# Kernel tuning notes

Hardware: AMD Instinct MI355X
Metric: run time of the kernel (lower is better)

Reference implementation:

```python
import jax, jax.numpy as jnp
import numpy as np

B, SEQ, NVAR, DM, K = 2, 512, 64, 128, 2
SCALE = DM ** -0.5  # ScaledDotProductAttention scale, lsa=False so constant


def _period_branch(x4, Wel, bel, Wq, bq, Wk, bk, Wv, bv, Wo, bo, period):
    # x4: [B, DM(time), NVAR, DM(dim)] -- output of start_embed
    pad = (-DM) % period
    pn = (DM + pad) // period  # period_num
    xp = jnp.pad(x4, ((0, 0), (0, pad), (0, 0), (0, 0)))
    # torch .unfold(dim=1, size=period, step=period) -> [B, pn, NVAR, DM, period]
    xw = xp.reshape(B, pn, period, NVAR, DM).transpose(0, 1, 3, 4, 2)
    # emb_linear over the d_model (dim) axis
    xw = jnp.einsum('bqndl,ed->bqnel', xw, Wel) + bel[None, None, None, :, None]
    # -> [B, NVAR, dim, pn, period] then flatten to conv1d layout [bn, dim, L]
    X = xw.transpose(0, 2, 3, 1, 4).reshape(B * NVAR, DM, pn * period)
    # 1x1 Conv1d QKV projections over the channel (dim) axis
    q = jnp.einsum('bdl,ed->bel', X, Wq) + bq[None, :, None]
    k = jnp.einsum('bdl,ed->bel', X, Wk) + bk[None, :, None]
    v = jnp.einsum('bdl,ed->bel', X, Wv) + bv[None, :, None]
    q_s = q.reshape(B * NVAR, DM, pn, period).transpose(0, 1, 3, 2)  # [bn,dim,pl,pn]
    k_s = k.reshape(B * NVAR, DM, pn, period)                         # [bn,dim,pn,pl]
    v_s = v.reshape(B * NVAR, DM, pn, period).transpose(0, 1, 3, 2)  # [bn,dim,pl,pn]
    attn = jax.nn.softmax(jnp.einsum('bdip,bdpj->bdij', q_s, k_s) * SCALE, axis=-1)
    o = jnp.einsum('bdij,bdjp->bdip', attn, v_s)  # [bn, dim, period, pn]
    o = o.reshape(B * NVAR, DM, period * pn)[:, :, :DM]  # truncate to n_heads=DM
    return o @ Wo.T + bo  # to_out Linear(n_heads, n_heads), dropout eval-mode


def reference(x, W_emb, b_emb, W_start, b_start, Wel, bel, Wq, bq, Wk, bk, Wv, bv, Wo, bo, f1, f2):
    # inverted embedding: Linear(seq_len->d_model) over time, then permute -> [B, DM, NVAR]
    xe = (jnp.einsum('bsn,sd->bnd', x, W_emb) + b_emb).transpose(0, 2, 1)
    # FFT_for_Period amplitudes; top-k frequency indices f1,f2 are static (host-side in torch)
    amp = jnp.abs(jnp.fft.rfft(xe, axis=1)).mean(-1)  # [B, DM//2+1]
    pw = jax.nn.softmax(jnp.stack([amp[:, f1], amp[:, f2]], -1), axis=-1)  # [B, K]
    # start_embed: Linear(1 -> d_model) -> [B, DM, NVAR, DM]
    x4 = xe[..., None] * W_start + b_start
    outs = [_period_branch(x4, Wel, bel, Wq, bq, Wk, bk, Wv, bv, Wo, bo, DM // f)
            for f in (f1, f2)]
    res = jnp.stack(outs, -1)                      # [B*NVAR, DM, DM, K]
    pw_b = jnp.repeat(pw, NVAR, axis=0)            # [B*NVAR, K] (b-major order matches reshape)
    out = (res * pw_b[:, None, None, :]).sum(-1)
    return out.reshape(B, NVAR, DM, DM)


def setup_inputs() -> dict:
    key = jax.random.key(0)
    ks = jax.random.split(key, 16)
    s = 0.02
    d = {
        'x': jax.random.normal(ks[0], (B, SEQ, NVAR), jnp.float32),
        'W_emb': jax.random.normal(ks[1], (SEQ, DM), jnp.float32) * s,
        'b_emb': jax.random.normal(ks[2], (DM,), jnp.float32) * s,
        'W_start': jax.random.normal(ks[3], (DM,), jnp.float32) * s,
        'b_start': jax.random.normal(ks[4], (DM,), jnp.float32) * s,
        'Wel': jax.random.normal(ks[5], (DM, DM), jnp.float32) * s,
        'bel': jax.random.normal(ks[6], (DM,), jnp.float32) * s,
        'Wq': jax.random.normal(ks[7], (DM, DM), jnp.float32) * s,
        'bq': jax.random.normal(ks[8], (DM,), jnp.float32) * s,
        'Wk': jax.random.normal(ks[9], (DM, DM), jnp.float32) * s,
        'bk': jax.random.normal(ks[10], (DM,), jnp.float32) * s,
        'Wv': jax.random.normal(ks[11], (DM, DM), jnp.float32) * s,
        'bv': jax.random.normal(ks[12], (DM,), jnp.float32) * s,
        'Wo': jax.random.normal(ks[13], (DM, DM), jnp.float32) * s,
        'bo': jax.random.normal(ks[14], (DM,), jnp.float32) * s,
    }
    # host-side FFT period detection, mirroring torch's .detach().cpu().numpy() topk
    xe = np.einsum('bsn,sd->bnd', np.asarray(d['x']), np.asarray(d['W_emb'])) + np.asarray(d['b_emb'])
    xe = xe.transpose(0, 2, 1)  # [B, DM, NVAR]
    fl = np.abs(np.fft.rfft(xe, axis=1)).mean(0).mean(-1)
    fl[0] = 0.0
    top = np.argsort(-fl, kind='stable')[:K]
    d['f1'] = int(top[0])
    d['f2'] = int(top[1])
    return d
```

## Files before the change

kernel.cpp:

```cpp
#include <hip/hip_runtime.h>

#define DMD 128
#define NV 64
#define BB 2
#define SQ 512
#define NBN 128
#define ASCALE 0.08838834764831845f
#define L2E 1.4426950408889634f
#define CSC (ASCALE * L2E)

#define WS_XE  0
#define WS_PW  (WS_XE + NBN*DMD)
#define WS_VEC (WS_PW + 4)
#define WS_OB  (WS_VEC + 9*DMD)

__global__ __launch_bounds__(512) void k_xe(const float* __restrict__ x,
                                            const float* __restrict__ W_emb,
                                            const float* __restrict__ b_emb,
                                            float* __restrict__ ws) {
    int bn = blockIdx.x;
    int b = bn >> 6, n = bn & 63;
    int tid = threadIdx.x;
    int t = tid & 127, sc = tid >> 7;
    __shared__ float xsh[SQ];
    __shared__ float part[3][DMD];
    xsh[tid] = x[(b * SQ + tid) * NV + n];
    __syncthreads();
    float acc = 0.f;
    const float* W = W_emb + (sc * 128) * DMD + t;
#pragma unroll 8
    for (int s = 0; s < 128; ++s) acc = fmaf(xsh[sc * 128 + s], W[s * DMD], acc);
    if (sc) part[sc - 1][t] = acc;
    __syncthreads();
    if (sc == 0)
        ws[WS_XE + bn * DMD + t] = acc + part[0][t] + part[1][t] + part[2][t] + b_emb[t];
}

__global__ __launch_bounds__(128) void k_prep(const int* __restrict__ f1p,
                                              const int* __restrict__ f2p,
                                              const float* __restrict__ Wel, const float* __restrict__ bel,
                                              const float* __restrict__ W_start, const float* __restrict__ b_start,
                                              const float* __restrict__ Wq, const float* __restrict__ bq,
                                              const float* __restrict__ Wk, const float* __restrict__ bk,
                                              const float* __restrict__ Wv, const float* __restrict__ bv,
                                              float* __restrict__ ws) {
    int tid = threadIdx.x;
    __shared__ float ct[DMD], st[DMD];
    __shared__ float a2[2];
    __shared__ float A[DMD], C[DMD], BL[DMD];
    if (blockIdx.x < 2) {
        int b = blockIdx.x;
        float ang = (float)tid * 0.04908738521234052f;
        ct[tid] = cosf(ang);
        st[tid] = sinf(ang);
        __syncthreads();
        int k = tid >> 6;
        int n = tid & 63;
        int f = k ? f2p[0] : f1p[0];
        const float* xr = ws + WS_XE + (b * NV + n) * DMD;
        float re = 0.f, im = 0.f;
        for (int t = 0; t < DMD; ++t) {
            int ph = (f * t) & (DMD - 1);
            float v = xr[t];
            re = fmaf(v, ct[ph], re);
            im = fmaf(v, st[ph], im);
        }
        float amp = sqrtf(re * re + im * im);
        for (int off = 32; off > 0; off >>= 1) amp += __shfl_down(amp, off);
        if (n == 0) a2[k] = amp * (1.0f / NV);
        __syncthreads();
        if (tid == 0) {
            float m = fmaxf(a2[0], a2[1]);
            float e0 = expf(a2[0] - m), e1 = expf(a2[1] - m);
            float inv = 1.0f / (e0 + e1);
            ws[WS_PW + b * 2 + 0] = e0 * inv;
            ws[WS_PW + b * 2 + 1] = e1 * inv;
        }
    } else {
        int e = tid;
        float a = 0.f, c = 0.f;
        for (int d = 0; d < DMD; ++d) {
            float w = Wel[e * DMD + d];
            a = fmaf(w, W_start[d], a);
            c = fmaf(w, b_start[d], c);
        }
        A[e] = a;
        C[e] = c + bel[e];
        BL[e] = bel[e];
        __syncthreads();
        float aq = 0, cq = 0, pq = 0, ak = 0, ck = 0, pk = 0, av = 0, cv = 0, pv = 0;
        for (int d = 0; d < DMD; ++d) {
            float Ad = A[d], Cd = C[d], Bd = BL[d];
            float wq = Wq[e * DMD + d], wk = Wk[e * DMD + d], wv = Wv[e * DMD + d];
            aq = fmaf(wq, Ad, aq); cq = fmaf(wq, Cd, cq); pq = fmaf(wq, Bd, pq);
            ak = fmaf(wk, Ad, ak); ck = fmaf(wk, Cd, ck); pk = fmaf(wk, Bd, pk);
            av = fmaf(wv, Ad, av); cv = fmaf(wv, Cd, cv); pv = fmaf(wv, Bd, pv);
        }
        float* V = ws + WS_VEC;
        V[0 * DMD + e] = aq; V[1 * DMD + e] = cq + bq[e]; V[2 * DMD + e] = pq + bq[e];
        V[3 * DMD + e] = ak; V[4 * DMD + e] = ck + bk[e]; V[5 * DMD + e] = pk + bk[e];
        V[6 * DMD + e] = av; V[7 * DMD + e] = cv + bv[e]; V[8 * DMD + e] = pv + bv[e];
    }
}


template<int UH, int NP>
__device__ __forceinline__ void attn_pathA(
    int P, int pn, int r, int Prows, int e0, int br, float pwv,
    const float* __restrict__ V, const float* xs, const float* U,
    const float* xt, float (*obuf)[132], int tid)
{
    int lane4 = tid & 3;
    int i0 = tid >> 2;
    int jb = lane4 * UH;

    float Ur[UH], xtr[UH], xq0[UH], xq1[UH];
#pragma unroll
    for (int u = 0; u < UH; ++u) {
        int j = jb + u, jc = (j < P) ? j : 0;
        Ur[u] = U[jc];
        xtr[u] = xt[jc];
        xq0[u] = (j < DMD) ? xs[j] : 0.f;
        int i1 = P + j;
        xq1[u] = (i1 < DMD) ? xs[i1] : 0.f;
    }

    int nrep = (Prows > 32) ? 2 : 1;
    for (int rep = 0; rep < nrep; ++rep) {
        int i = i0 + rep * 32;
        bool rowact = (i < Prows);
        int ic = rowact ? i : 0;
        float xtic = xt[ic];
        bool rowvalid = (ic < r);

        float g[UH];
#pragma unroll
        for (int u = 0; u < UH; ++u) g[u] = 0.f;
        for (int p = 0; p < pn - 1; ++p) {
            float xi = xs[p * P + ic];
#pragma unroll
            for (int u = 0; u < UH; ++u) {
                int j = jb + u, jc = (j < P) ? j : 0;
                g[u] = fmaf(xi, xs[p * P + jc], g[u]);
            }
        }

        for (int ec = 0; ec < 8; ++ec) {
            int e = e0 + ec;
            float Aq = V[e],        Cq = V[DMD + e],   Pq = V[2 * DMD + e];
            float Ak = V[3 * DMD + e], Ck = V[4 * DMD + e], Pk = V[5 * DMD + e];
            float Av = V[6 * DMD + e], Cv = V[7 * DMD + e], Pv = V[8 * DMD + e];
            float c1 = CSC * Aq * Ak, c3 = CSC * Cq * Ak;
            float asi = CSC * (rowvalid ? fmaf(xtic, Aq, Cq) : Pq);

            float l0 = 0.f, l1 = 0.f, w0 = 0.f, w1 = 0.f;
            float accq[NP];
#pragma unroll
            for (int q = 0; q < NP; ++q) accq[q] = 0.f;

#pragma unroll
            for (int u = 0; u < UH; ++u) {
                int j = jb + u;
                float bK = (j < r) ? fmaf(xtr[u], Ak, Ck) : Pk;
                float S = fmaf(asi, bK, fmaf(c3, Ur[u], c1 * g[u]));
                float ev = exp2f(S);
                ev = (j < P) ? ev : 0.f;
                if (u & 1) l1 += ev; else l0 += ev;
                float evr = (j < r) ? ev : 0.f;
                if (u & 1) w1 += evr; else w0 += evr;
                accq[0] = fmaf(ev, xq0[u], accq[0]);
                if (NP >= 2) accq[1] = fmaf(ev, xq1[u], accq[1]);
#pragma unroll
                for (int q = 2; q < NP; ++q) {
                    int idx = q * P + j;
                    float xv = (idx < DMD) ? xs[idx] : 0.f;
                    accq[q] = fmaf(ev, xv, accq[q]);
                }
            }
            float l = l0 + l1, wr = w0 + w1;
            l += __shfl_xor(l, 1);  l += __shfl_xor(l, 2);
            wr += __shfl_xor(wr, 1); wr += __shfl_xor(wr, 2);
#pragma unroll
            for (int q = 0; q < NP; ++q) {
                if (q < pn) {
                    accq[q] += __shfl_xor(accq[q], 1);
                    accq[q] += __shfl_xor(accq[q], 2);
                }
            }
            if (lane4 == 0 && rowact) {
                float li = 1.f / l;
#pragma unroll
                for (int q = 0; q < NP; ++q) {
                    if (q < pn) {
                        int mo = i * pn + q;
                        if (mo < DMD) {
                            float o;
                            if (q == pn - 1) {
                                float sl = wr * li;
                                o = fmaf(Av, accq[q] * li, fmaf(Cv, sl, Pv * (1.f - sl)));
                            } else {
                                o = fmaf(Av, accq[q] * li, Cv);
                            }
                            float val = pwv * o;
                            if (br == 0) obuf[ec][mo] = val;
                            else         obuf[ec][mo] += val;
                        }
                    }
                }
            }
        }
    }
}

__device__ __forceinline__ void attn_pathB(
    int P, int pn, int r, int Prows, int e0, int br, float pwv,
    const float* __restrict__ V, const float* xs, const float* U,
    const float* xt, const float* G, float (*obuf)[132], int tid)
{
    int i2 = tid / pn, p2 = tid - i2 * pn;
    bool lastp = (p2 == pn - 1);
    bool rowvalid = (i2 < r);
    float xti = xt[i2];

    float Gr[16], xsr[16], Urr[16], xtr[16];
#pragma unroll
    for (int j = 0; j < 16; ++j) {
        int jc = (j < P) ? j : 0;
        Gr[j] = G[i2 * P + jc];
        Urr[j] = U[jc];
        xtr[j] = xt[jc];
        int idx = p2 * P + j;
        xsr[j] = (idx < DMD && j < P) ? xs[idx] : 0.f;
    }

    for (int ec = 0; ec < 8; ++ec) {
        int e = e0 + ec;
        float Aq = V[e],        Cq = V[DMD + e],   Pq = V[2 * DMD + e];
        float Ak = V[3 * DMD + e], Ck = V[4 * DMD + e], Pk = V[5 * DMD + e];
        float Av = V[6 * DMD + e], Cv = V[7 * DMD + e], Pv = V[8 * DMD + e];
        float c1 = CSC * Aq * Ak, c3 = CSC * Cq * Ak;
        float asi = CSC * (rowvalid ? fmaf(xti, Aq, Cq) : Pq);

        float l0 = 0.f, l1 = 0.f, w0 = 0.f, w1 = 0.f, a0 = 0.f, a1 = 0.f;
#pragma unroll
        for (int j = 0; j < 16; ++j) {
            float bK = (j < r) ? fmaf(xtr[j], Ak, Ck) : Pk;
            float S = fmaf(asi, bK, fmaf(c3, Urr[j], c1 * Gr[j]));
            float ev = exp2f(S);
            ev = (j < P) ? ev : 0.f;
            if (j & 1) l1 += ev; else l0 += ev;
            float evr = (j < r) ? ev : 0.f;
            if (j & 1) w1 += evr; else w0 += evr;
            if (j & 1) a1 = fmaf(ev, xsr[j], a1); else a0 = fmaf(ev, xsr[j], a0);
        }
        float l = l0 + l1, wr = w0 + w1, accx = a0 + a1;
        float li = 1.f / l;
        float o;
        if (lastp) { float sl = wr * li; o = fmaf(Av, accx * li, fmaf(Cv, sl, Pv * (1.f - sl))); }
        else       o = fmaf(Av, accx * li, Cv);
        float val = pwv * o;
        if (br == 0) obuf[ec][tid] = val;
        else         obuf[ec][tid] += val;
    }
}

__device__ __forceinline__ void attn_rank1(
    int e0, int br, float pwv, const float* __restrict__ V,
    const float* xs, float (*obuf)[132], int tid)
{
    float xi = xs[tid];
    float t[8], l[8], ax[8];
#pragma unroll
    for (int k = 0; k < 8; ++k) {
        int e = e0 + k;
        float Aq = V[e], Cq = V[DMD + e], Ak = V[3 * DMD + e];
        t[k] = CSC * fmaf(xi, Aq, Cq) * Ak;
        l[k] = 0.f; ax[k] = 0.f;
    }
#pragma unroll 4
    for (int j = 0; j < DMD; ++j) {
        float xj = xs[j];
#pragma unroll
        for (int k = 0; k < 8; ++k) {
            float ev = exp2f(t[k] * xj);
            l[k] += ev;
            ax[k] = fmaf(ev, xj, ax[k]);
        }
    }
#pragma unroll
    for (int k = 0; k < 8; ++k) {
        int e = e0 + k;
        float Av = V[6 * DMD + e], Cv = V[7 * DMD + e];
        float o = fmaf(Av, ax[k] / l[k], Cv);
        float val = pwv * o;
        if (br == 0) obuf[k][tid] = val;
        else         obuf[k][tid] += val;
    }
}

__global__ __launch_bounds__(128) void k_attn(const int* __restrict__ f1p,
                                              const int* __restrict__ f2p,
                                              float* __restrict__ ws) {
    int bn = blockIdx.y;
    int b = bn >> 6;
    int e0 = blockIdx.x * 8;
    int tid = threadIdx.x;

    __shared__ float xs[DMD], U[64], xt[64], G[256];
    __shared__ float obuf[8][132];

    xs[tid] = ws[WS_XE + bn * DMD + tid];
    int fv0 = f1p[0], fv1 = f2p[0];
    float pw0 = ws[WS_PW + b * 2 + 0];
    float pw1 = ws[WS_PW + b * 2 + 1];
    const float* V = ws + WS_VEC;
    __syncthreads();

    for (int br = 0; br < 2; ++br) {
        int f = br ? fv1 : fv0;
        float pwv = br ? pw1 : pw0;
        int P = DMD / f;
        int pn = (DMD + P - 1) / P;
        int r = DMD - (pn - 1) * P;
        int Prows = (DMD + pn - 1) / pn;

        if (br == 1) __syncthreads();

        if (P == DMD) {
            attn_rank1(e0, br, pwv, V, xs, obuf, tid);
        } else {
            if (tid < P) {
                float s = 0.f;
                for (int p = 0; p < pn - 1; ++p) s += xs[p * P + tid];
                U[tid] = s;
                xt[tid] = (tid < r) ? xs[(pn - 1) * P + tid] : 0.f;
            }
            if (P <= 16) {
                int tot = Prows * P;
                for (int idx = tid; idx < tot; idx += 128) {
                    int gi = idx / P, gj = idx - gi * P;
                    float s = 0.f;
                    for (int p = 0; p < pn - 1; ++p)
                        s = fmaf(xs[p * P + gi], xs[p * P + gj], s);
                    G[idx] = s;
                }
            }
            __syncthreads();

            if (P > 32) {
                if (pn == 2) attn_pathA<16, 2>(P, pn, r, Prows, e0, br, pwv, V, xs, U, xt, obuf, tid);
                else         attn_pathA<16, 4>(P, pn, r, Prows, e0, br, pwv, V, xs, U, xt, obuf, tid);
            } else if (P > 16) {
                attn_pathA<8, 8>(P, pn, r, Prows, e0, br, pwv, V, xs, U, xt, obuf, tid);
            } else {
                attn_pathB(P, pn, r, Prows, e0, br, pwv, V, xs, U, xt, G, obuf, tid);
            }
        }
    }
    __syncthreads();
    for (int ec = 0; ec < 8; ++ec)
        ws[WS_OB + (bn * DMD + e0 + ec) * DMD + tid] = obuf[ec][tid];
}

__global__ __launch_bounds__(256) void k_out(const float* __restrict__ Wo,
                                             const float* __restrict__ bo,
                                             const float* __restrict__ ws,
                                             float* __restrict__ out) {
    int blk = blockIdx.x;
    int bn0 = (blk >> 2) * 2;
    int e0  = (blk & 3) * 32;
    int tid = threadIdx.x;
    __shared__ __align__(16) float WTc[32 * 132];
    __shared__ __align__(16) float oT[2][32][36];
    int hg = tid & 31, eg = tid >> 5, h0 = hg * 4;

    float acc[2][4][4];
#pragma unroll
    for (int a = 0; a < 2; ++a)
#pragma unroll
        for (int c = 0; c < 4; ++c)
#pragma unroll
            for (int d = 0; d < 4; ++d) acc[a][c][d] = 0.f;

    for (int mc = 0; mc < 4; ++mc) {
        int m0 = mc * 32;
        __syncthreads();
        for (int idx = tid; idx < 4096; idx += 256) {
            int h = idx >> 5, mm = idx & 31;
            WTc[mm * 132 + h] = Wo[h * DMD + m0 + mm];
        }
        for (int idx = tid; idx < 2048; idx += 256) {
            int bnl = idx >> 10, rem = idx & 1023, e = rem >> 5, mm = rem & 31;
            oT[bnl][mm][e] = ws[WS_OB + ((bn0 + bnl) * DMD + e0 + e) * DMD + m0 + mm];
        }
        __syncthreads();
#pragma unroll 4
        for (int mm = 0; mm < 32; ++mm) {
            const float4 wv = *reinterpret_cast<const float4*>(&WTc[mm * 132 + h0]);
            const float4 q0 = *reinterpret_cast<const float4*>(&oT[0][mm][eg * 4]);
            const float4 q1 = *reinterpret_cast<const float4*>(&oT[1][mm][eg * 4]);
            float ae[2][4] = {{q0.x, q0.y, q0.z, q0.w}, {q1.x, q1.y, q1.z, q1.w}};
#pragma unroll
            for (int bnl = 0; bnl < 2; ++bnl) {
#pragma unroll
                for (int el = 0; el < 4; ++el) {
                    float a = ae[bnl][el];
                    acc[bnl][el][0] = fmaf(a, wv.x, acc[bnl][el][0]);
                    acc[bnl][el][1] = fmaf(a, wv.y, acc[bnl][el][1]);
                    acc[bnl][el][2] = fmaf(a, wv.z, acc[bnl][el][2]);
                    acc[bnl][el][3] = fmaf(a, wv.w, acc[bnl][el][3]);
                }
            }
        }
    }
    const float4 bov = *reinterpret_cast<const float4*>(&bo[h0]);
#pragma unroll
    for (int bnl = 0; bnl < 2; ++bnl) {
#pragma unroll
        for (int el = 0; el < 4; ++el) {
            float4 res = { acc[bnl][el][0] + bov.x, acc[bnl][el][1] + bov.y,
                           acc[bnl][el][2] + bov.z, acc[bnl][el][3] + bov.w };
            int e = e0 + eg * 4 + el;
            *reinterpret_cast<float4*>(&out[((bn0 + bnl) * DMD + e) * DMD + h0]) = res;
        }
    }
}

extern "C" void kernel_launch(void* const* d_in, const int* in_sizes, int n_in,
                              void* d_out, int out_size, void* d_ws, size_t ws_size,
                              hipStream_t stream) {
    const float* x       = (const float*)d_in[0];
    const float* W_emb   = (const float*)d_in[1];
    const float* b_emb   = (const float*)d_in[2];
    const float* W_start = (const float*)d_in[3];
    const float* b_start = (const float*)d_in[4];
    const float* Wel     = (const float*)d_in[5];
    const float* bel     = (const float*)d_in[6];
    const float* Wq      = (const float*)d_in[7];
    const float* bq      = (const float*)d_in[8];
    const float* Wk      = (const float*)d_in[9];
    const float* bk      = (const float*)d_in[10];
    const float* Wv      = (const float*)d_in[11];
    const float* bv      = (const float*)d_in[12];
    const float* Wo      = (const float*)d_in[13];
    const float* bo      = (const float*)d_in[14];
    const int*   f1p     = (const int*)d_in[15];
    const int*   f2p     = (const int*)d_in[16];
    float* ws  = (float*)d_ws;
    float* out = (float*)d_out;

    k_xe<<<NBN, 512, 0, stream>>>(x, W_emb, b_emb, ws);
    k_prep<<<3, 128, 0, stream>>>(f1p, f2p, Wel, bel, W_start, b_start,
                                  Wq, bq, Wk, bk, Wv, bv, ws);
    k_attn<<<dim3(16, NBN), 128, 0, stream>>>(f1p, f2p, ws);
    k_out<<<256, 256, 0, stream>>>(Wo, bo, ws, out);
}
```

Baseline: 91.55 us.

## Split attention over more blocks, add specialized power-of-two and small-period paths

Each attention block now handles 4 output channels instead of 8, doubling the grid to 32x128 blocks. The per-channel vectors are staged into shared memory once per block. New specialized paths handle exact power-of-two periods (no remainder handling, shuffle reductions) and small periods, where score weights are computed once per channel into shared memory and then reduced per row. The aim is more parallelism and less redundant score work, at the cost of more blocks repeating the Gram/U setup and extra barriers in the small-period path.

Result: faster. 81.95 us (-10.5%).

```diff
diff --git a/kernel.cpp b/kernel.cpp
--- a/kernel.cpp
+++ b/kernel.cpp
@@ -104,10 +104,201 @@
 }
 
 
+__device__ __forceinline__ void attn_rank1(int br, float pwv, const float (*Vsh)[4],
+                                           const float* xs, float (*obuf)[132], int tid) {
+    float xi = xs[tid];
+    float t[4], l[4], ax[4];
+#pragma unroll
+    for (int k = 0; k < 4; ++k) {
+        float Aq = Vsh[0][k], Cq = Vsh[1][k], Ak = Vsh[3][k];
+        t[k] = CSC * fmaf(xi, Aq, Cq) * Ak;
+        l[k] = 0.f; ax[k] = 0.f;
+    }
+#pragma unroll 4
+    for (int j = 0; j < DMD; ++j) {
+        float xj = xs[j];
+#pragma unroll
+        for (int k = 0; k < 4; ++k) {
+            float ev = exp2f(t[k] * xj);
+            l[k] += ev;
+            ax[k] = fmaf(ev, xj, ax[k]);
+        }
+    }
+#pragma unroll
+    for (int k = 0; k < 4; ++k) {
+        float Av = Vsh[6][k], Cv = Vsh[7][k];
+        float o = fmaf(Av, ax[k] / l[k], Cv);
+        float val = pwv * o;
+        if (br == 0) obuf[k][tid] = val; else obuf[k][tid] += val;
+    }
+}
+
+template<int PP, int NP>
+__device__ __forceinline__ void attn_pow2(int br, float pwv, const float (*Vsh)[4],
+                                          const float* xs, float (*obuf)[132], int tid) {
+    const int UH = PP / 4;
+    int lane4 = tid & 3, i0 = tid >> 2, jb = lane4 * UH;
+
+    float xq[NP][UH], U2[UH];
+#pragma unroll
+    for (int u = 0; u < UH; ++u) {
+        int j = jb + u;
+        float s = 0.f;
+#pragma unroll
+        for (int q = 0; q < NP; ++q) { float xv = xs[q * PP + j]; xq[q][u] = xv; s += xv; }
+        U2[u] = s;
+    }
+    const int NREP = (PP == 64) ? 2 : 1;
+#pragma unroll
+    for (int rep = 0; rep < NREP; ++rep) {
+        int i = i0 + rep * 32;
+        float G2[UH];
+#pragma unroll
+        for (int u = 0; u < UH; ++u) G2[u] = 0.f;
+#pragma unroll
+        for (int q = 0; q < NP; ++q) {
+            float xi = xs[q * PP + i];
+#pragma unroll
+            for (int u = 0; u < UH; ++u) G2[u] = fmaf(xi, xq[q][u], G2[u]);
+        }
+        for (int ec = 0; ec < 4; ++ec) {
+            float Aq = Vsh[0][ec], Cq = Vsh[1][ec];
+            float Ak = Vsh[3][ec];
+            float Av = Vsh[6][ec], Cv = Vsh[7][ec];
+            float t = CSC * Ak;
+            float d1 = t * Aq, d2 = t * Cq;
+            float l0 = 0.f, l1 = 0.f;
+            float accq[NP];
+#pragma unroll
+            for (int q = 0; q < NP; ++q) accq[q] = 0.f;
+#pragma unroll
+            for (int u = 0; u < UH; ++u) {
+                float ev = exp2f(fmaf(d1, G2[u], d2 * U2[u]));
+                if (u & 1) l1 += ev; else l0 += ev;
+#pragma unroll
+                for (int q = 0; q < NP; ++q) accq[q] = fmaf(ev, xq[q][u], accq[q]);
+            }
+            float l = l0 + l1;
+            l += __shfl_xor(l, 1); l += __shfl_xor(l, 2);
+#pragma unroll
+            for (int q = 0; q < NP; ++q) {
+                accq[q] += __shfl_xor(accq[q], 1);
+                accq[q] += __shfl_xor(accq[q], 2);
+            }
+            if (lane4 == 0) {
+                float li = 1.f / l;
+#pragma unroll
+                for (int q = 0; q < NP; ++q) {
+                    float o = fmaf(Av, accq[q] * li, Cv);
+                    float val = pwv * o;
+                    int mo = i * NP + q;
+                    if (br == 0) obuf[ec][mo] = val; else obuf[ec][mo] += val;
+                }
+            }
+        }
+    }
+}
+
+template<int UB>
+__device__ __forceinline__ void attn_small(
+    int P, int pn, int r, int Prows, int br, float pwv,
+    const float (*Vsh)[4], const float* xs, const float* U, const float* xt,
+    float* W, float (*obuf)[132], int tid)
+{
+    int GP = P + 1;
+    int tot = Prows * P;
+    unsigned mP = (4096u + (unsigned)P - 1u) / (unsigned)P;
+    unsigned mpn = (4096u + (unsigned)pn - 1u) / (unsigned)pn;
+
+    bool v0 = (tid < tot);
+    int i0 = (int)(((unsigned)tid * mP) >> 12);
+    int j0 = tid - i0 * P;
+    bool A0 = (i0 < r), c0 = (j0 < r);
+    float xtj0 = xt[j0], Uj0 = U[j0];
+    float xti0 = A0 ? xt[i0] : 0.f;
+    float g0 = 0.f;
+    for (int p = 0; p < pn - 1; ++p) g0 = fmaf(xs[p * P + i0], xs[p * P + j0], g0);
+    float Gx0 = (A0 && c0) ? fmaf(xti0, xtj0, g0) : g0;
+    float Ux0 = (A0 && c0) ? Uj0 + xtj0 : Uj0;
+    float Xw0 = (!A0 && c0) ? xtj0 : 0.f;
+    float mw0 = c0 ? 1.f : 0.f;
+    int wa0 = i0 * GP + j0;
+
+    int idx1 = tid + 128;
+    bool v1 = (idx1 < tot);
+    int idx1c = v1 ? idx1 : 0;
+    int i1 = (int)(((unsigned)idx1c * mP) >> 12);
+    int j1 = idx1c - i1 * P;
+    bool A1 = (i1 < r), c1 = (j1 < r);
+    float xtj1 = xt[j1], Uj1 = U[j1];
+    float xti1 = A1 ? xt[i1] : 0.f;
+    float g1 = 0.f;
+    for (int p = 0; p < pn - 1; ++p) g1 = fmaf(xs[p * P + i1], xs[p * P + j1], g1);
+    float Gx1 = (A1 && c1) ? fmaf(xti1, xtj1, g1) : g1;
+    float Ux1 = (A1 && c1) ? Uj1 + xtj1 : Uj1;
+    float Xw1 = (!A1 && c1) ? xtj1 : 0.f;
+    float mw1 = c1 ? 1.f : 0.f;
+    int wa1 = i1 * GP + j1;
+
+    int i2 = (int)(((unsigned)tid * mpn) >> 12);
+    int p2 = tid - i2 * pn;
+    bool lastp = (p2 == pn - 1);
+    int row2 = i2 * GP;
+    float xsr[UB];
+#pragma unroll
+    for (int j = 0; j < UB; ++j) {
+        int idx = p2 * P + j;
+        xsr[j] = (j < P && idx < DMD) ? xs[idx] : 0.f;
+    }
+
+    for (int ec = 0; ec < 4; ++ec) {
+        float Aq = Vsh[0][ec], Cq = Vsh[1][ec], Pq = Vsh[2][ec];
+        float Ak = Vsh[3][ec], Ck = Vsh[4][ec], Pk = Vsh[5][ec];
+        float Av = Vsh[6][ec], Cv = Vsh[7][ec], Pv = Vsh[8][ec];
+        float t = CSC * Ak;
+        float d1 = t * Aq, d2 = t * Cq, d3 = t * Pq;
+        float ckpk = CSC * (Ck - Pk);
+
+        if (v0) {
+            float aS = A0 ? fmaf(Aq, xti0, Cq) : Pq;
+            float S = (ckpk * aS) * mw0;
+            S = fmaf(d3, Xw0, S);
+            S = fmaf(d2, Ux0, S);
+            S = fmaf(d1, Gx0, S);
+            W[wa0] = exp2f(S);
+        }
+        if (v1) {
+            float aS = A1 ? fmaf(Aq, xti1, Cq) : Pq;
+            float S = (ckpk * aS) * mw1;
+            S = fmaf(d3, Xw1, S);
+            S = fmaf(d2, Ux1, S);
+            S = fmaf(d1, Gx1, S);
+            W[wa1] = exp2f(S);
+        }
+        __syncthreads();
+        float l = 0.f, wr = 0.f, ax = 0.f;
+#pragma unroll
+        for (int j = 0; j < UB; ++j) {
+            float w = W[row2 + ((j < P) ? j : 0)];
+            w = (j < P) ? w : 0.f;
+            l += w;
+            wr += (j < r) ? w : 0.f;
+            ax = fmaf(w, xsr[j], ax);
+        }
+        float li = 1.f / l;
+        float o;
+        if (lastp) { float sl = wr * li; o = fmaf(Av, ax * li, fmaf(Cv, sl, Pv * (1.f - sl))); }
+        else       o = fmaf(Av, ax * li, Cv);
+        float val = pwv * o;
+        if (br == 0) obuf[ec][tid] = val; else obuf[ec][tid] += val;
+        __syncthreads();
+    }
+}
+
 template<int UH, int NP>
-__device__ __forceinline__ void attn_pathA(
-    int P, int pn, int r, int Prows, int e0, int br, float pwv,
-    const float* __restrict__ V, const float* xs, const float* U,
+__device__ __forceinline__ void attn_midA(
+    int P, int pn, int r, int Prows, int br, float pwv,
+    const float (*Vsh)[4], const float* xs, const float* U,
     const float* xt, float (*obuf)[132], int tid)
 {
     int lane4 = tid & 3;
@@ -121,10 +312,9 @@
         Ur[u] = U[jc];
         xtr[u] = xt[jc];
         xq0[u] = (j < DMD) ? xs[j] : 0.f;
-        int i1 = P + j;
-        xq1[u] = (i1 < DMD) ? xs[i1] : 0.f;
-    }
-
+        int i1x = P + j;
+        xq1[u] = (i1x < DMD) ? xs[i1x] : 0.f;
+    }
     int nrep = (Prows > 32) ? 2 : 1;
     for (int rep = 0; rep < nrep; ++rep) {
         int i = i0 + rep * 32;
@@ -132,7 +322,6 @@
         int ic = rowact ? i : 0;
         float xtic = xt[ic];
         bool rowvalid = (ic < r);
-
         float g[UH];
 #pragma unroll
         for (int u = 0; u < UH; ++u) g[u] = 0.f;
@@ -144,12 +333,10 @@
                 g[u] = fmaf(xi, xs[p * P + jc], g[u]);
             }
         }
-
-        for (int ec = 0; ec < 8; ++ec) {
-            int e = e0 + ec;
-            float Aq = V[e],        Cq = V[DMD + e],   Pq = V[2 * DMD + e];
-            float Ak = V[3 * DMD + e], Ck = V[4 * DMD + e], Pk = V[5 * DMD + e];
-            float Av = V[6 * DMD + e], Cv = V[7 * DMD + e], Pv = V[8 * DMD + e];
+        for (int ec = 0; ec < 4; ++ec) {
+            float Aq = Vsh[0][ec], Cq = Vsh[1][ec], Pq = Vsh[2][ec];
+            float Ak = Vsh[3][ec], Ck = Vsh[4][ec], Pk = Vsh[5][ec];
+            float Av = Vsh[6][ec], Cv = Vsh[7][ec], Pv = Vsh[8][ec];
             float c1 = CSC * Aq * Ak, c3 = CSC * Cq * Ak;
             float asi = CSC * (rowvalid ? fmaf(xtic, Aq, Cq) : Pq);
 
@@ -157,7 +344,6 @@
             float accq[NP];
 #pragma unroll
             for (int q = 0; q < NP; ++q) accq[q] = 0.f;
-
 #pragma unroll
             for (int u = 0; u < UH; ++u) {
                 int j = jb + u;
@@ -212,108 +398,23 @@
     }
 }
 
-__device__ __forceinline__ void attn_pathB(
-    int P, int pn, int r, int Prows, int e0, int br, float pwv,
-    const float* __restrict__ V, const float* xs, const float* U,
-    const float* xt, const float* G, float (*obuf)[132], int tid)
-{
-    int i2 = tid / pn, p2 = tid - i2 * pn;
-    bool lastp = (p2 == pn - 1);
-    bool rowvalid = (i2 < r);
-    float xti = xt[i2];
-
-    float Gr[16], xsr[16], Urr[16], xtr[16];
-#pragma unroll
-    for (int j = 0; j < 16; ++j) {
-        int jc = (j < P) ? j : 0;
-        Gr[j] = G[i2 * P + jc];
-        Urr[j] = U[jc];
-        xtr[j] = xt[jc];
-        int idx = p2 * P + j;
-        xsr[j] = (idx < DMD && j < P) ? xs[idx] : 0.f;
-    }
-
-    for (int ec = 0; ec < 8; ++ec) {
-        int e = e0 + ec;
-        float Aq = V[e],        Cq = V[DMD + e],   Pq = V[2 * DMD + e];
-        float Ak = V[3 * DMD + e], Ck = V[4 * DMD + e], Pk = V[5 * DMD + e];
-        float Av = V[6 * DMD + e], Cv = V[7 * DMD + e], Pv = V[8 * DMD + e];
-        float c1 = CSC * Aq * Ak, c3 = CSC * Cq * Ak;
-        float asi = CSC * (rowvalid ? fmaf(xti, Aq, Cq) : Pq);
-
-        float l0 = 0.f, l1 = 0.f, w0 = 0.f, w1 = 0.f, a0 = 0.f, a1 = 0.f;
-#pragma unroll
-        for (int j = 0; j < 16; ++j) {
-            float bK = (j < r) ? fmaf(xtr[j], Ak, Ck) : Pk;
-            float S = fmaf(asi, bK, fmaf(c3, Urr[j], c1 * Gr[j]));
-            float ev = exp2f(S);
-            ev = (j < P) ? ev : 0.f;
-            if (j & 1) l1 += ev; else l0 += ev;
-            float evr = (j < r) ? ev : 0.f;
-            if (j & 1) w1 += evr; else w0 += evr;
-            if (j & 1) a1 = fmaf(ev, xsr[j], a1); else a0 = fmaf(ev, xsr[j], a0);
-        }
-        float l = l0 + l1, wr = w0 + w1, accx = a0 + a1;
-        float li = 1.f / l;
-        float o;
-        if (lastp) { float sl = wr * li; o = fmaf(Av, accx * li, fmaf(Cv, sl, Pv * (1.f - sl))); }
-        else       o = fmaf(Av, accx * li, Cv);
-        float val = pwv * o;
-        if (br == 0) obuf[ec][tid] = val;
-        else         obuf[ec][tid] += val;
-    }
-}
-
-__device__ __forceinline__ void attn_rank1(
-    int e0, int br, float pwv, const float* __restrict__ V,
-    const float* xs, float (*obuf)[132], int tid)
-{
-    float xi = xs[tid];
-    float t[8], l[8], ax[8];
-#pragma unroll
-    for (int k = 0; k < 8; ++k) {
-        int e = e0 + k;
-        float Aq = V[e], Cq = V[DMD + e], Ak = V[3 * DMD + e];
-        t[k] = CSC * fmaf(xi, Aq, Cq) * Ak;
-        l[k] = 0.f; ax[k] = 0.f;
-    }
-#pragma unroll 4
-    for (int j = 0; j < DMD; ++j) {
-        float xj = xs[j];
-#pragma unroll
-        for (int k = 0; k < 8; ++k) {
-            float ev = exp2f(t[k] * xj);
-            l[k] += ev;
-            ax[k] = fmaf(ev, xj, ax[k]);
-        }
-    }
-#pragma unroll
-    for (int k = 0; k < 8; ++k) {
-        int e = e0 + k;
-        float Av = V[6 * DMD + e], Cv = V[7 * DMD + e];
-        float o = fmaf(Av, ax[k] / l[k], Cv);
-        float val = pwv * o;
-        if (br == 0) obuf[k][tid] = val;
-        else         obuf[k][tid] += val;
-    }
-}
-
 __global__ __launch_bounds__(128) void k_attn(const int* __restrict__ f1p,
                                               const int* __restrict__ f2p,
                                               float* __restrict__ ws) {
-    int bn = blockIdx.y;
-    int b = bn >> 6;
-    int e0 = blockIdx.x * 8;
+    int bn = blockIdx.y, b = bn >> 6;
+    int e0 = blockIdx.x * 4;
     int tid = threadIdx.x;
 
-    __shared__ float xs[DMD], U[64], xt[64], G[256];
-    __shared__ float obuf[8][132];
+    __shared__ float xs[DMD], U[64], xt[64];
+    __shared__ float Vsh[9][4];
+    __shared__ float W[288];
+    __shared__ float obuf[4][132];
 
     xs[tid] = ws[WS_XE + bn * DMD + tid];
+    if (tid < 36) Vsh[tid >> 2][tid & 3] = ws[WS_VEC + (tid >> 2) * DMD + e0 + (tid & 3)];
     int fv0 = f1p[0], fv1 = f2p[0];
     float pw0 = ws[WS_PW + b * 2 + 0];
     float pw1 = ws[WS_PW + b * 2 + 1];
-    const float* V = ws + WS_VEC;
     __syncthreads();
 
     for (int br = 0; br < 2; ++br) {
@@ -327,7 +428,7 @@
         if (br == 1) __syncthreads();
 
         if (P == DMD) {
-            attn_rank1(e0, br, pwv, V, xs, obuf, tid);
+            attn_rank1(br, pwv, Vsh, xs, obuf, tid);
         } else {
             if (tid < P) {
                 float s = 0.f;
@@ -335,30 +436,18 @@
                 U[tid] = s;
                 xt[tid] = (tid < r) ? xs[(pn - 1) * P + tid] : 0.f;
             }
-            if (P <= 16) {
-                int tot = Prows * P;
-                for (int idx = tid; idx < tot; idx += 128) {
-                    int gi = idx / P, gj = idx - gi * P;
-                    float s = 0.f;
-                    for (int p = 0; p < pn - 1; ++p)
-                        s = fmaf(xs[p * P + gi], xs[p * P + gj], s);
-                    G[idx] = s;
-                }
-            }
             __syncthreads();
-
-            if (P > 32) {
-                if (pn == 2) attn_pathA<16, 2>(P, pn, r, Prows, e0, br, pwv, V, xs, U, xt, obuf, tid);
-                else         attn_pathA<16, 4>(P, pn, r, Prows, e0, br, pwv, V, xs, U, xt, obuf, tid);
-            } else if (P > 16) {
-                attn_pathA<8, 8>(P, pn, r, Prows, e0, br, pwv, V, xs, U, xt, obuf, tid);
-            } else {
-                attn_pathB(P, pn, r, Prows, e0, br, pwv, V, xs, U, xt, G, obuf, tid);
-            }
+            if (P <= 4)       attn_small<4>(P, pn, r, Prows, br, pwv, Vsh, xs, U, xt, W, obuf, tid);
+            else if (P <= 8)  attn_small<8>(P, pn, r, Prows, br, pwv, Vsh, xs, U, xt, W, obuf, tid);
+            else if (P <= 16) attn_small<16>(P, pn, r, Prows, br, pwv, Vsh, xs, U, xt, W, obuf, tid);
+            else if (P == 64) attn_pow2<64, 2>(br, pwv, Vsh, xs, obuf, tid);
+            else if (P == 32) attn_pow2<32, 4>(br, pwv, Vsh, xs, obuf, tid);
+            else if (P > 32)  attn_midA<16, 4>(P, pn, r, Prows, br, pwv, Vsh, xs, U, xt, obuf, tid);
+            else              attn_midA<8, 8>(P, pn, r, Prows, br, pwv, Vsh, xs, U, xt, obuf, tid);
         }
     }
     __syncthreads();
-    for (int ec = 0; ec < 8; ++ec)
+    for (int ec = 0; ec < 4; ++ec)
         ws[WS_OB + (bn * DMD + e0 + ec) * DMD + tid] = obuf[ec][tid];
 }
 
@@ -452,6 +541,6 @@
     k_xe<<<NBN, 512, 0, stream>>>(x, W_emb, b_emb, ws);
     k_prep<<<3, 128, 0, stream>>>(f1p, f2p, Wel, bel, W_start, b_start,
                                   Wq, bq, Wk, bk, Wv, bv, ws);
-    k_attn<<<dim3(16, NBN), 128, 0, stream>>>(f1p, f2p, ws);
+    k_attn<<<dim3(32, NBN), 128, 0, stream>>>(f1p, f2p, ws);
     k_out<<<256, 256, 0, stream>>>(Wo, bo, ws, out);
 }
```
